# Kernel optimization log

Measured on AMD Instinct MI355X. Metric: run time of the kernel, lower is better.

The kernel has to match this reference:

```python
import jax, jax.numpy as jnp
import numpy as np

B, N, F, H, F_ = 4, 2048, 64, 4, 64


def setup_inputs() -> dict:
    key = jax.random.key(0)
    kx, ka, kw, ks, kn = jax.random.split(key, 5)
    X = jax.random.normal(kx, (B, N, F), dtype=jnp.float32)
    A = (jax.random.uniform(ka, (B, N, N)) < 0.05).astype(jnp.float32)
    A = jnp.maximum(A, jnp.eye(N, dtype=jnp.float32)[None])
    W = jax.random.normal(kw, (H, F, F_), dtype=jnp.float32) * 0.1
    a_self = jax.random.normal(ks, (H, F_), dtype=jnp.float32) * 0.1
    a_neigh = jax.random.normal(kn, (H, F_), dtype=jnp.float32) * 0.1
    return {"X": X, "A": A, "W": W, "a_self": a_self, "a_neigh": a_neigh}


def reference(X, A, W, a_self, a_neigh):
    # linear transform per head: [B,H,N,F_]
    lin = jnp.einsum('bnf,hfo->bhno', X, W)
    # additive attention scores
    s_self = jnp.einsum('bhno,ho->bhn', lin, a_self)[:, :, :, None]   # [B,H,N,1]
    s_neigh = jnp.einsum('bhno,ho->bhn', lin, a_neigh)[:, :, None, :]  # [B,H,1,N]
    dense = s_self + s_neigh                                           # [B,H,N,N]
    dense = jnp.where(dense >= 0, dense, 0.2 * dense)                  # LeakyReLU(0.2)
    BIG = jnp.float32(1e10)
    mask = jnp.exp(A * -BIG) * -BIG                                    # 0 where edge, -1e10 where no edge
    logits = dense + mask[:, None, :, :]
    attn = jax.nn.softmax(logits, axis=-1)
    # dropout is identity at inference (attn_dropout=0.0)
    feats = jnp.einsum('bhnm,bhmo->bhno', attn, lin)                   # [B,H,N,F_]
    feats = jax.nn.relu(feats)                                         # activation before concat
    b, h, n, f_ = feats.shape
    out = feats.transpose(0, 2, 1, 3).reshape(b, n, h * f_)            # concat heads
    return out
```

## Files before the change

kernel.cpp:

```cpp
#include <hip/hip_runtime.h>

#define BB 4
#define NN 2048
#define FF 64
#define HH 4
#define FO 64
#define CAP 256

typedef unsigned short ushort_t;


__global__ __launch_bounds__(256) void BatchGraphAttention_84378927497895_kernel(
    const float* __restrict__ W, const float* __restrict__ a_self,
    const float* __restrict__ a_neigh, float* __restrict__ w_self,
    float* __restrict__ w_neigh) {
  int t = threadIdx.x;
  int h = t >> 6;
  const float* Wp = W + t * FO;
  const float* as = a_self + h * FO;
  const float* an = a_neigh + h * FO;
  float acc_s = 0.f, acc_n = 0.f;
#pragma unroll
  for (int o = 0; o < FO; ++o) {
    float w = Wp[o];
    acc_s += w * as[o];
    acc_n += w * an[o];
  }
  w_self[t] = acc_s;
  w_neigh[t] = acc_n;
}

__global__ __launch_bounds__(256) void BatchGraphAttention_84378927497895_kernel2(
    const float* __restrict__ X, const float* __restrict__ w_self,
    const float* __restrict__ w_neigh, const float* __restrict__ W,
    float* __restrict__ WT2, float* __restrict__ s_self4,
    float* __restrict__ s_neigh4) {
  int t = threadIdx.x, lane = t & 63, wv = t >> 6;
  int bn = blockIdx.x * 4 + wv;
  int g = lane & 15;
  int h = lane >> 4;
  float4 x = ((const float4*)X)[(size_t)bn * 16 + g];
  float4 ws = ((const float4*)w_self)[h * 16 + g];
  float4 wn = ((const float4*)w_neigh)[h * 16 + g];
  float vs = x.x * ws.x + x.y * ws.y + x.z * ws.z + x.w * ws.w;
  float vn = x.x * wn.x + x.y * wn.y + x.z * wn.z + x.w * wn.w;
#pragma unroll
  for (int off = 1; off < 16; off <<= 1) {
    vs += __shfl_xor(vs, off, 64);
    vn += __shfl_xor(vn, off, 64);
  }
  if (g == 0) {
    s_self4[bn * 4 + h] = vs;
    s_neigh4[bn * 4 + h] = vn;
  }
  if (blockIdx.x < 16) {
    int gg = blockIdx.x;
    int hh = t >> 6, o = t & 63;
    const float* Wb = W + (size_t)(hh * FF) * FO + o;
    float4 wt;
    wt.x = Wb[(4 * gg + 0) * FO];
    wt.y = Wb[(4 * gg + 1) * FO];
    wt.z = Wb[(4 * gg + 2) * FO];
    wt.w = Wb[(4 * gg + 3) * FO];
    ((float4*)WT2)[(hh * 16 + gg) * 64 + o] = wt;
  }
}

__global__ __launch_bounds__(256, 8) void BatchGraphAttention_84378927497895_kernel3(
    const float* __restrict__ A, const float* __restrict__ X,
    const float* __restrict__ WT2, const float* __restrict__ s_self4,
    const float* __restrict__ s_neigh4, float* __restrict__ out) {
  __shared__ float4 plt[4][CAP];
  __shared__ ushort_t idxs[4][CAP];
  int t = threadIdx.x, lane = t & 63, wv = t >> 6;
  int bn = blockIdx.x * 4 + wv;
  int b = bn >> 11;
  float4* pl = plt[wv];
  ushort_t* idx = idxs[wv];

  const float4* Ar = (const float4*)(A + (size_t)bn * NN);
  unsigned long long lt = (1ull << lane) - 1ull;
  int cnt = 0;
#pragma unroll
  for (int r = 0; r < 8; ++r) {
    float4 av = Ar[r * 64 + lane];
    unsigned c = (unsigned)((r * 64 + lane) * 4);
    unsigned long long m0 = __ballot(av.x != 0.f);
    if (av.x != 0.f) { int p = cnt + (int)__popcll(m0 & lt); if (p < CAP) idx[p] = (ushort_t)c; }
    cnt += (int)__popcll(m0);
    unsigned long long m1 = __ballot(av.y != 0.f);
    if (av.y != 0.f) { int p = cnt + (int)__popcll(m1 & lt); if (p < CAP) idx[p] = (ushort_t)(c + 1); }
    cnt += (int)__popcll(m1);
    unsigned long long m2 = __ballot(av.z != 0.f);
    if (av.z != 0.f) { int p = cnt + (int)__popcll(m2 & lt); if (p < CAP) idx[p] = (ushort_t)(c + 2); }
    cnt += (int)__popcll(m2);
    unsigned long long m3 = __ballot(av.w != 0.f);
    if (av.w != 0.f) { int p = cnt + (int)__popcll(m3 & lt); if (p < CAP) idx[p] = (ushort_t)(c + 3); }
    cnt += (int)__popcll(m3);
  }
  cnt = __builtin_amdgcn_readfirstlane(cnt);
  if (cnt > CAP) cnt = CAP;
  int pcnt = (cnt + 3) & ~3;

  float4 ss = ((const float4*)s_self4)[bn];
  const float4* sn = ((const float4*)s_neigh4) + (size_t)b * NN;
  float4 sum = make_float4(0.f, 0.f, 0.f, 0.f);
#define EXP_GAT(K)                                                          \
  {                                                                         \
    int j = lane + K * 64;                                                  \
    if (j < cnt) {                                                          \
      int m = idx[j];                                                       \
      float4 s = sn[m];                                                     \
      float4 lg;                                                            \
      lg.x = ss.x + s.x; lg.y = ss.y + s.y;                                 \
      lg.z = ss.z + s.z; lg.w = ss.w + s.w;                                 \
      lg.x = (lg.x >= 0.f) ? lg.x : 0.2f * lg.x;                            \
      lg.y = (lg.y >= 0.f) ? lg.y : 0.2f * lg.y;                            \
      lg.z = (lg.z >= 0.f) ? lg.z : 0.2f * lg.z;                            \
      lg.w = (lg.w >= 0.f) ? lg.w : 0.2f * lg.w;                            \
      float4 e;                                                             \
      e.x = __expf(lg.x); e.y = __expf(lg.y);                               \
      e.z = __expf(lg.z); e.w = __expf(lg.w);                               \
      sum.x += e.x; sum.y += e.y; sum.z += e.z; sum.w += e.w;               \
      pl[j] = e;                                                            \
    } else if (j < pcnt) {                                                  \
      pl[j] = make_float4(0.f, 0.f, 0.f, 0.f);                              \
      idx[j] = 0;             \
    }                                                                       \
  }
  EXP_GAT(0) EXP_GAT(1) EXP_GAT(2) EXP_GAT(3)
#undef EXP_GAT

  int q = lane >> 4;
  int g = lane & 15;
  const float4* xq = (const float4*)(X + (size_t)b * (NN * FF)) + g;
  int shamt = (q & 1) * 16;
  bool hi = (q & 2) != 0;
  float4 acc0 = make_float4(0.f, 0.f, 0.f, 0.f);
  float4 acc1 = acc0, acc2 = acc0, acc3 = acc0;
  {
    uint2 pk = *(const uint2*)idx;
    unsigned pw = hi ? pk.y : pk.x;
    int m = (pw >> shamt) & 0xffff;
    float4 xv = xq[m * 16];
    for (int j = 0; j < pcnt; j += 4) {
      int jn = (j + 4 < pcnt) ? (j + 4) : 0;
      uint2 pk2 = *(const uint2*)(idx + jn);
      unsigned pw2 = hi ? pk2.y : pk2.x;
      int m2 = (pw2 >> shamt) & 0xffff;
      float4 xv2 = xq[m2 * 16];
      float4 p = pl[j + q];
      acc0.x += xv.x * p.x; acc0.y += xv.y * p.x; acc0.z += xv.z * p.x; acc0.w += xv.w * p.x;
      acc1.x += xv.x * p.y; acc1.y += xv.y * p.y; acc1.z += xv.z * p.y; acc1.w += xv.w * p.y;
      acc2.x += xv.x * p.z; acc2.y += xv.y * p.z; acc2.z += xv.z * p.z; acc2.w += xv.w * p.z;
      acc3.x += xv.x * p.w; acc3.y += xv.y * p.w; acc3.z += xv.z * p.w; acc3.w += xv.w * p.w;
      xv = xv2;
    }
  }
#define XRED(v)                                                             \
  v.x += __shfl_xor(v.x, 16, 64); v.y += __shfl_xor(v.y, 16, 64);           \
  v.z += __shfl_xor(v.z, 16, 64); v.w += __shfl_xor(v.w, 16, 64);           \
  v.x += __shfl_xor(v.x, 32, 64); v.y += __shfl_xor(v.y, 32, 64);           \
  v.z += __shfl_xor(v.z, 32, 64); v.w += __shfl_xor(v.w, 32, 64);
  XRED(acc0) XRED(acc1) XRED(acc2) XRED(acc3)
#undef XRED

#pragma unroll
  for (int off = 1; off < 64; off <<= 1) {
    sum.x += __shfl_xor(sum.x, off, 64);
    sum.y += __shfl_xor(sum.y, off, 64);
    sum.z += __shfl_xor(sum.z, off, 64);
    sum.w += __shfl_xor(sum.w, off, 64);
  }
  float4 sv;
  sv.x = 1.f / sum.x; sv.y = 1.f / sum.y; sv.z = 1.f / sum.z; sv.w = 1.f / sum.w;

  {
    float* ysr = (float*)pl;
    if (lane < 16) {
      ((float4*)(ysr + 0 * FF))[g] = make_float4(acc0.x * sv.x, acc0.y * sv.x, acc0.z * sv.x, acc0.w * sv.x);
      ((float4*)(ysr + 1 * FF))[g] = make_float4(acc1.x * sv.y, acc1.y * sv.y, acc1.z * sv.y, acc1.w * sv.y);
      ((float4*)(ysr + 2 * FF))[g] = make_float4(acc2.x * sv.z, acc2.y * sv.z, acc2.z * sv.z, acc2.w * sv.z);
      ((float4*)(ysr + 3 * FF))[g] = make_float4(acc3.x * sv.w, acc3.y * sv.w, acc3.z * sv.w, acc3.w * sv.w);
    }
  }
  __syncthreads();

  {
    const float4* wtp = (const float4*)WT2 + (size_t)(wv * 16) * 64 + lane;
    const float4* yr0 = (const float4*)((const float*)plt[0] + wv * FF);
    const float4* yr1 = (const float4*)((const float*)plt[1] + wv * FF);
    const float4* yr2 = (const float4*)((const float*)plt[2] + wv * FF);
    const float4* yr3 = (const float4*)((const float*)plt[3] + wv * FF);
    float o0 = 0.f, o1 = 0.f, o2 = 0.f, o3 = 0.f;
#pragma unroll 4
    for (int gg = 0; gg < 16; ++gg) {
      float4 wt = wtp[gg * 64];
      float4 a0 = yr0[gg];
      float4 a1 = yr1[gg];
      float4 a2 = yr2[gg];
      float4 a3 = yr3[gg];
      o0 += a0.x * wt.x + a0.y * wt.y + a0.z * wt.z + a0.w * wt.w;
      o1 += a1.x * wt.x + a1.y * wt.y + a1.z * wt.z + a1.w * wt.w;
      o2 += a2.x * wt.x + a2.y * wt.y + a2.z * wt.z + a2.w * wt.w;
      o3 += a3.x * wt.x + a3.y * wt.y + a3.z * wt.z + a3.w * wt.w;
    }
    size_t ob = (size_t)(blockIdx.x * 4) * (HH * FO) + wv * FO + lane;
    out[ob + 0 * (HH * FO)] = fmaxf(o0, 0.f);
    out[ob + 1 * (HH * FO)] = fmaxf(o1, 0.f);
    out[ob + 2 * (HH * FO)] = fmaxf(o2, 0.f);
    out[ob + 3 * (HH * FO)] = fmaxf(o3, 0.f);
  }
}

extern "C" void kernel_launch(void* const* d_in, const int* in_sizes, int n_in,
                              void* d_out, int out_size, void* d_ws,
                              size_t ws_size, hipStream_t stream) {
  const float* X = (const float*)d_in[0];
  const float* A = (const float*)d_in[1];
  const float* W = (const float*)d_in[2];
  const float* a_self = (const float*)d_in[3];
  const float* a_neigh = (const float*)d_in[4];
  float* out = (float*)d_out;

  float* w_self = (float*)d_ws;
  float* w_neigh = w_self + HH * FF;
  float* s_self4 = w_neigh + HH * FF;
  float* s_neigh4 = s_self4 + (size_t)BB * NN * HH;
  float* WT2 = s_neigh4 + (size_t)BB * NN * HH;

  BatchGraphAttention_84378927497895_kernel<<<1, 256, 0, stream>>>(
      W, a_self, a_neigh, w_self, w_neigh);
  BatchGraphAttention_84378927497895_kernel2<<<BB * NN / 4, 256, 0, stream>>>(
      X, w_self, w_neigh, W, WT2, s_self4, s_neigh4);
  BatchGraphAttention_84378927497895_kernel3<<<BB * NN / 4, 256, 0, stream>>>(
      A, X, WT2, s_self4, s_neigh4, out);
}
```

Measured before the change: 129.3 us.

## Move adjacency compaction into the score kernel and pass neighbor lists via global memory

The per-row scan of the adjacency matrix (ballot/popcount compaction into neighbor indices) moves from the aggregation kernel into the score kernel. Compacted indices and counts go to workspace in global memory, and the aggregation kernel reads them there instead of from shared memory. This shortens the aggregation kernel and drops its shared index buffer, which may help occupancy and latency hiding. In exchange it adds global writes and reads of the index lists, and the neighbor gathers now read indices from global/L2 rather than LDS. The dominant A read still happens once, just in a different kernel.

```diff
diff --git a/kernel.cpp b/kernel.cpp
--- a/kernel.cpp
+++ b/kernel.cpp
@@ -33,26 +33,61 @@
 __global__ __launch_bounds__(256) void BatchGraphAttention_84378927497895_kernel2(
     const float* __restrict__ X, const float* __restrict__ w_self,
     const float* __restrict__ w_neigh, const float* __restrict__ W,
-    float* __restrict__ WT2, float* __restrict__ s_self4,
-    float* __restrict__ s_neigh4) {
+    const float* __restrict__ A, float* __restrict__ WT2,
+    float* __restrict__ s_self4, float* __restrict__ s_neigh4,
+    ushort_t* __restrict__ idxg, int* __restrict__ cntg) {
   int t = threadIdx.x, lane = t & 63, wv = t >> 6;
   int bn = blockIdx.x * 4 + wv;
-  int g = lane & 15;
-  int h = lane >> 4;
-  float4 x = ((const float4*)X)[(size_t)bn * 16 + g];
-  float4 ws = ((const float4*)w_self)[h * 16 + g];
-  float4 wn = ((const float4*)w_neigh)[h * 16 + g];
-  float vs = x.x * ws.x + x.y * ws.y + x.z * ws.z + x.w * ws.w;
-  float vn = x.x * wn.x + x.y * wn.y + x.z * wn.z + x.w * wn.w;
-#pragma unroll
-  for (int off = 1; off < 16; off <<= 1) {
-    vs += __shfl_xor(vs, off, 64);
-    vn += __shfl_xor(vn, off, 64);
-  }
-  if (g == 0) {
-    s_self4[bn * 4 + h] = vs;
-    s_neigh4[bn * 4 + h] = vn;
-  }
+
+  const float4* Ar = (const float4*)(A + (size_t)bn * NN);
+  float4 av[8];
+#pragma unroll
+  for (int r = 0; r < 8; ++r) av[r] = Ar[r * 64 + lane];
+
+  {
+    int g = lane & 15;
+    int h = lane >> 4;
+    float4 x = ((const float4*)X)[(size_t)bn * 16 + g];
+    float4 ws = ((const float4*)w_self)[h * 16 + g];
+    float4 wn = ((const float4*)w_neigh)[h * 16 + g];
+    float vs = x.x * ws.x + x.y * ws.y + x.z * ws.z + x.w * ws.w;
+    float vn = x.x * wn.x + x.y * wn.y + x.z * wn.z + x.w * wn.w;
+#pragma unroll
+    for (int off = 1; off < 16; off <<= 1) {
+      vs += __shfl_xor(vs, off, 64);
+      vn += __shfl_xor(vn, off, 64);
+    }
+    if (g == 0) {
+      s_self4[bn * 4 + h] = vs;
+      s_neigh4[bn * 4 + h] = vn;
+    }
+  }
+
+  ushort_t* ig = idxg + (size_t)bn * CAP;
+  unsigned long long lt = (1ull << lane) - 1ull;
+  int cnt = 0;
+#pragma unroll
+  for (int r = 0; r < 8; ++r) {
+    unsigned c = (unsigned)((r * 64 + lane) * 4);
+    unsigned long long m0 = __ballot(av[r].x != 0.f);
+    if (av[r].x != 0.f) { int p = cnt + (int)__popcll(m0 & lt); if (p < CAP) ig[p] = (ushort_t)c; }
+    cnt += (int)__popcll(m0);
+    unsigned long long m1 = __ballot(av[r].y != 0.f);
+    if (av[r].y != 0.f) { int p = cnt + (int)__popcll(m1 & lt); if (p < CAP) ig[p] = (ushort_t)(c + 1); }
+    cnt += (int)__popcll(m1);
+    unsigned long long m2 = __ballot(av[r].z != 0.f);
+    if (av[r].z != 0.f) { int p = cnt + (int)__popcll(m2 & lt); if (p < CAP) ig[p] = (ushort_t)(c + 2); }
+    cnt += (int)__popcll(m2);
+    unsigned long long m3 = __ballot(av[r].w != 0.f);
+    if (av[r].w != 0.f) { int p = cnt + (int)__popcll(m3 & lt); if (p < CAP) ig[p] = (ushort_t)(c + 3); }
+    cnt += (int)__popcll(m3);
+  }
+  int cs = __builtin_amdgcn_readfirstlane(cnt);
+  if (cs > CAP) cs = CAP;
+  int pc = (cs + 3) & ~3;
+  if (lane < pc - cs) ig[cs + lane] = 0;
+  if (lane == 0) cntg[bn] = cs;
+
   if (blockIdx.x < 16) {
     int gg = blockIdx.x;
     int hh = t >> 6, o = t & 63;
@@ -67,39 +102,18 @@
 }
 
 __global__ __launch_bounds__(256, 8) void BatchGraphAttention_84378927497895_kernel3(
-    const float* __restrict__ A, const float* __restrict__ X,
-    const float* __restrict__ WT2, const float* __restrict__ s_self4,
-    const float* __restrict__ s_neigh4, float* __restrict__ out) {
+    const ushort_t* __restrict__ idxg, const int* __restrict__ cntg,
+    const float* __restrict__ X, const float* __restrict__ WT2,
+    const float* __restrict__ s_self4, const float* __restrict__ s_neigh4,
+    float* __restrict__ out) {
   __shared__ float4 plt[4][CAP];
-  __shared__ ushort_t idxs[4][CAP];
   int t = threadIdx.x, lane = t & 63, wv = t >> 6;
   int bn = blockIdx.x * 4 + wv;
   int b = bn >> 11;
   float4* pl = plt[wv];
-  ushort_t* idx = idxs[wv];
-
-  const float4* Ar = (const float4*)(A + (size_t)bn * NN);
-  unsigned long long lt = (1ull << lane) - 1ull;
-  int cnt = 0;
-#pragma unroll
-  for (int r = 0; r < 8; ++r) {
-    float4 av = Ar[r * 64 + lane];
-    unsigned c = (unsigned)((r * 64 + lane) * 4);
-    unsigned long long m0 = __ballot(av.x != 0.f);
-    if (av.x != 0.f) { int p = cnt + (int)__popcll(m0 & lt); if (p < CAP) idx[p] = (ushort_t)c; }
-    cnt += (int)__popcll(m0);
-    unsigned long long m1 = __ballot(av.y != 0.f);
-    if (av.y != 0.f) { int p = cnt + (int)__popcll(m1 & lt); if (p < CAP) idx[p] = (ushort_t)(c + 1); }
-    cnt += (int)__popcll(m1);
-    unsigned long long m2 = __ballot(av.z != 0.f);
-    if (av.z != 0.f) { int p = cnt + (int)__popcll(m2 & lt); if (p < CAP) idx[p] = (ushort_t)(c + 2); }
-    cnt += (int)__popcll(m2);
-    unsigned long long m3 = __ballot(av.w != 0.f);
-    if (av.w != 0.f) { int p = cnt + (int)__popcll(m3 & lt); if (p < CAP) idx[p] = (ushort_t)(c + 3); }
-    cnt += (int)__popcll(m3);
-  }
-  cnt = __builtin_amdgcn_readfirstlane(cnt);
-  if (cnt > CAP) cnt = CAP;
+  const ushort_t* idx = idxg + (size_t)bn * CAP;
+
+  int cnt = __builtin_amdgcn_readfirstlane(cntg[bn]);
   int pcnt = (cnt + 3) & ~3;
 
   float4 ss = ((const float4*)s_self4)[bn];
@@ -125,7 +139,6 @@
       pl[j] = e;                                                            \
     } else if (j < pcnt) {                                                  \
       pl[j] = make_float4(0.f, 0.f, 0.f, 0.f);                              \
-      idx[j] = 0;             \
     }                                                                       \
   }
   EXP_GAT(0) EXP_GAT(1) EXP_GAT(2) EXP_GAT(3)
@@ -228,11 +241,13 @@
   float* s_self4 = w_neigh + HH * FF;
   float* s_neigh4 = s_self4 + (size_t)BB * NN * HH;
   float* WT2 = s_neigh4 + (size_t)BB * NN * HH;
+  int* cntg = (int*)(WT2 + (size_t)HH * FF * FO);
+  ushort_t* idxg = (ushort_t*)(cntg + BB * NN);
 
   BatchGraphAttention_84378927497895_kernel<<<1, 256, 0, stream>>>(
       W, a_self, a_neigh, w_self, w_neigh);
   BatchGraphAttention_84378927497895_kernel2<<<BB * NN / 4, 256, 0, stream>>>(
-      X, w_self, w_neigh, W, WT2, s_self4, s_neigh4);
+      X, w_self, w_neigh, W, A, WT2, s_self4, s_neigh4, idxg, cntg);
   BatchGraphAttention_84378927497895_kernel3<<<BB * NN / 4, 256, 0, stream>>>(
-      A, X, WT2, s_self4, s_neigh4, out);
-}
+      idxg, cntg, X, WT2, s_self4, s_neigh4, out);
+}
```

New measurement: 138.5 us. 7.1% more time.
